# Optimization experiments

Hardware: AMD Instinct MI355X
Metric: run time of the kernel (lower is better)

The kernel has to match this reference:

```python
import jax, jax.numpy as jnp
import numpy as np

NUM_HEADS = 32
NUM_KV_HEADS = 8
HEAD_DIM = 128
SCALE = 1.0 / np.sqrt(HEAD_DIM)
BATCH = 16
MAX_CTX = 2048
NUM_SLOTS = BATCH * MAX_CTX + BATCH  # 32784; last BATCH slots are the write targets


def setup_inputs() -> dict:
    key = jax.random.key(0)
    ks = jax.random.split(key, 8)
    q = jax.random.normal(ks[0], (BATCH, NUM_HEADS, HEAD_DIM), dtype=jnp.float32)
    k = jax.random.normal(ks[1], (BATCH, NUM_KV_HEADS, HEAD_DIM), dtype=jnp.float32)
    v = jax.random.normal(ks[2], (BATCH, NUM_KV_HEADS, HEAD_DIM), dtype=jnp.float32)
    k_cache = jax.random.normal(ks[3], (NUM_SLOTS, NUM_KV_HEADS, HEAD_DIM), dtype=jnp.float32)
    v_cache = jax.random.normal(ks[4], (NUM_SLOTS, NUM_KV_HEADS, HEAD_DIM), dtype=jnp.float32)
    # each decode token writes its new kv into a fresh slot at the end of the pool
    slot_mapping = (BATCH * MAX_CTX + jnp.arange(BATCH)).astype(jnp.int64)
    # sparse-controller-selected active slots per request (paged, irregular)
    active_slots = jax.random.randint(ks[5], (BATCH, MAX_CTX), 0, NUM_SLOTS).astype(jnp.int64)
    # make the current token's slot the last active slot of its own request
    active_slots = active_slots.at[:, -1].set(slot_mapping)
    context_lens = jax.random.randint(ks[6], (BATCH,), 1, MAX_CTX + 1).astype(jnp.int64)
    return {
        "q": q, "k": k, "v": v,
        "k_cache": k_cache, "v_cache": v_cache,
        "slot_mapping": slot_mapping,
        "active_slots": active_slots,
        "context_lens": context_lens,
    }


def _attend(q, k, v, k_cache, v_cache, slot_mapping, active_slots, context_lens):
    # store_kvcache: scatter new k/v into flat slot cache; slot == -1 is skipped
    safe_slots = jnp.where(slot_mapping < 0, NUM_SLOTS, slot_mapping)  # OOB -> dropped
    kc = k_cache.at[safe_slots].set(k, mode="drop")
    vc = v_cache.at[safe_slots].set(v, mode="drop")

    # paged gather of the per-request active KV pages
    K = kc[active_slots]  # [B, L, Hkv, D]
    V = vc[active_slots]  # [B, L, Hkv, D]

    B, H, D = q.shape
    G = H // NUM_KV_HEADS  # GQA group size
    qg = q.reshape(B, NUM_KV_HEADS, G, D)

    # flash-decode stage1+stage2 == numerically-stable softmax attention over active slots
    scores = jnp.einsum("bkgd,blkd->bkgl", qg, K) * SCALE  # [B, Hkv, G, L]
    valid = jnp.arange(active_slots.shape[1])[None, :] < context_lens[:, None]  # [B, L]
    scores = jnp.where(valid[:, None, None, :], scores, jnp.float32(-1e30))
    p = jax.nn.softmax(scores, axis=-1)
    o = jnp.einsum("bkgl,blkd->bkgd", p, V).reshape(B, H, D)
    return o


def reference(q, k, v, k_cache, v_cache, slot_mapping, active_slots, context_lens):
    return _attend(q, k, v, k_cache, v_cache, slot_mapping, active_slots, context_lens)
```

## Files before the change

### kernel.cpp

```cpp
#include <hip/hip_runtime.h>
#include <hip/hip_bf16.h>
#include <float.h>

#define B 16
#define H 32
#define HKV 8
#define G 4
#define D 128
#define LMAX 2048
#define SCALE 0.08838834764831844f

template <int NSPLIT>
__global__ __launch_bounds__(256) void attn_partial(
    const float* __restrict__ q,
    const float* __restrict__ kin,
    const float* __restrict__ vin,
    const float* __restrict__ kc,
    const float* __restrict__ vc,
    const int*  __restrict__ slot_mapping,
    const int*  __restrict__ active_slots,
    const int*  __restrict__ context_lens,
    float* __restrict__ part_o,
    float* __restrict__ part_ml)
{
    constexpr int CHUNK = LMAX / NSPLIT;
    const int tid = threadIdx.x;
    int idx = blockIdx.x;
    const int split = idx % NSPLIT; idx /= NSPLIT;
    const int h = idx % HKV;
    const int b = idx / HKV;

    const int ctx   = context_lens[b];
    const int start = split * CHUNK;
    int nvalid = ctx - start;
    if (nvalid > CHUNK) nvalid = CHUNK;

    const size_t pbase = ((size_t)(b * HKV + h) * NSPLIT + split) * G;

    if (nvalid <= 0) {
        if (tid < G * 2) part_ml[pbase * 2 + tid] = (tid & 1) ? 0.f : -FLT_MAX;
        return;
    }

    __shared__ float sc[G][CHUNK];
    __shared__ const float* vptr[CHUNK];
    __shared__ float red[G][D];
    __shared__ int   sm[16];

    if (tid < 16) sm[tid] = slot_mapping[tid];
    __syncthreads();

    const int grp   = tid >> 3;
    const int lane8 = tid & 7;

    float4 qv[G][4];
#pragma unroll
    for (int g = 0; g < G; ++g) {
        const float* qp = q + ((size_t)(b * H + h * G + g)) * D;
#pragma unroll
        for (int i = 0; i < 4; ++i) {
            float4 t = *(const float4*)(qp + i * 32 + lane8 * 4);
            qv[g][i] = make_float4(t.x * SCALE, t.y * SCALE, t.z * SCALE, t.w * SCALE);
        }
    }

    const int iters = (nvalid + 31) >> 5;
    for (int it = 0; it < iters; ++it) {
        const int li = it * 32 + grp;
        if (li < nvalid) {
            const int l = start + li;
            const int s = active_slots[b * LMAX + l];
            int ov = -1;
#pragma unroll
            for (int j = 0; j < 16; ++j)
                if (sm[j] == s) ov = j;
            const float* kb = (ov >= 0) ? (kin + ((size_t)ov * HKV + h) * D)
                                        : (kc  + ((size_t)s  * HKV + h) * D);
            float pd0 = 0.f, pd1 = 0.f, pd2 = 0.f, pd3 = 0.f;
#pragma unroll
            for (int i = 0; i < 4; ++i) {
                float4 kv = *(const float4*)(kb + i * 32 + lane8 * 4);
                pd0 += kv.x * qv[0][i].x + kv.y * qv[0][i].y + kv.z * qv[0][i].z + kv.w * qv[0][i].w;
                pd1 += kv.x * qv[1][i].x + kv.y * qv[1][i].y + kv.z * qv[1][i].z + kv.w * qv[1][i].w;
                pd2 += kv.x * qv[2][i].x + kv.y * qv[2][i].y + kv.z * qv[2][i].z + kv.w * qv[2][i].w;
                pd3 += kv.x * qv[3][i].x + kv.y * qv[3][i].y + kv.z * qv[3][i].z + kv.w * qv[3][i].w;
            }
#pragma unroll
            for (int msk = 1; msk < 8; msk <<= 1) {
                pd0 += __shfl_xor(pd0, msk, 8);
                pd1 += __shfl_xor(pd1, msk, 8);
                pd2 += __shfl_xor(pd2, msk, 8);
                pd3 += __shfl_xor(pd3, msk, 8);
            }
            if (lane8 == 0) {
                sc[0][li] = pd0; sc[1][li] = pd1; sc[2][li] = pd2; sc[3][li] = pd3;
                vptr[li] = (ov >= 0) ? (vin + ((size_t)ov * HKV + h) * D)
                                     : (vc  + ((size_t)s  * HKV + h) * D);
            }
        }
    }
    __syncthreads();

    {
        const int g    = tid >> 6;
        const int lane = tid & 63;
        float m = -FLT_MAX;
        for (int i = lane; i < nvalid; i += 64) m = fmaxf(m, sc[g][i]);
#pragma unroll
        for (int msk = 1; msk < 64; msk <<= 1) m = fmaxf(m, __shfl_xor(m, msk, 64));
        float sum = 0.f;
        for (int i = lane; i < nvalid; i += 64) {
            float p = __expf(sc[g][i] - m);
            sc[g][i] = p;
            sum += p;
        }
#pragma unroll
        for (int msk = 1; msk < 64; msk <<= 1) sum += __shfl_xor(sum, msk, 64);
        if (lane == 0) {
            part_ml[(pbase + g) * 2 + 0] = m;
            part_ml[(pbase + g) * 2 + 1] = sum;
        }
    }
    __syncthreads();

    {
        const int dd   = tid & 127;
        const int half = tid >> 7;
        float a0 = 0.f, a1 = 0.f, a2 = 0.f, a3 = 0.f;
#pragma unroll 4
        for (int i = half; i < nvalid; i += 2) {
            const float* vb = vptr[i];
            const float vval = vb[dd];
            a0 += sc[0][i] * vval;
            a1 += sc[1][i] * vval;
            a2 += sc[2][i] * vval;
            a3 += sc[3][i] * vval;
        }
        if (half == 1) {
            red[0][dd] = a0; red[1][dd] = a1; red[2][dd] = a2; red[3][dd] = a3;
        }
        __syncthreads();
        if (half == 0) {
            part_o[(pbase + 0) * D + dd] = a0 + red[0][dd];
            part_o[(pbase + 1) * D + dd] = a1 + red[1][dd];
            part_o[(pbase + 2) * D + dd] = a2 + red[2][dd];
            part_o[(pbase + 3) * D + dd] = a3 + red[3][dd];
        }
    }
}

__global__ __launch_bounds__(128) void attn_reduce(
    const float* __restrict__ part_o,
    const float* __restrict__ part_ml,
    float* __restrict__ out,
    int nsplit)
{
    int idx = blockIdx.x;
    const int g = idx & 3;
    const int h = (idx >> 2) & 7;
    const int b = idx >> 5;
    const int d = threadIdx.x;

    const size_t base = (size_t)(b * HKV + h) * nsplit;

    float M = -FLT_MAX;
    for (int s = 0; s < nsplit; ++s) {
        const float l = part_ml[((base + s) * G + g) * 2 + 1];
        if (l > 0.f) M = fmaxf(M, part_ml[((base + s) * G + g) * 2 + 0]);
    }
    float L = 0.f, acc = 0.f;
    for (int s = 0; s < nsplit; ++s) {
        const float l = part_ml[((base + s) * G + g) * 2 + 1];
        if (l > 0.f) {
            const float e = __expf(part_ml[((base + s) * G + g) * 2 + 0] - M);
            L += l * e;
            acc += e * part_o[((base + s) * G + g) * D + d];
        }
    }
    out[((size_t)(b * H) + h * G + g) * D + d] = acc / (L > 0.f ? L : 1.f);
}

extern "C" void kernel_launch(void* const* d_in, const int* in_sizes, int n_in,
                              void* d_out, int out_size, void* d_ws, size_t ws_size,
                              hipStream_t stream) {
    const float* q  = (const float*)d_in[0];
    const float* k  = (const float*)d_in[1];
    const float* v  = (const float*)d_in[2];
    const float* kc = (const float*)d_in[3];
    const float* vc = (const float*)d_in[4];
    const int* slot_mapping = (const int*)d_in[5];
    const int* active_slots = (const int*)d_in[6];
    const int* context_lens = (const int*)d_in[7];
    float* out = (float*)d_out;

    const size_t need16 = ((size_t)B * HKV * 16 * G * D + (size_t)B * HKV * 16 * G * 2) * sizeof(float);
    const int nsplit = (ws_size >= need16) ? 16 : 8;

    float* part_o  = (float*)d_ws;
    float* part_ml = part_o + (size_t)B * HKV * nsplit * G * D;

    if (nsplit == 16) {
        attn_partial<16><<<B * HKV * 16, 256, 0, stream>>>(
            q, k, v, kc, vc, slot_mapping, active_slots, context_lens, part_o, part_ml);
    } else {
        attn_partial<8><<<B * HKV * 8, 256, 0, stream>>>(
            q, k, v, kc, vc, slot_mapping, active_slots, context_lens, part_o, part_ml);
    }
    attn_reduce<<<B * HKV * G, 128, 0, stream>>>(part_o, part_ml, out, nsplit);
}
```

Baseline: 48.57 us.

## Precompute slot pointers, vectorize PV accumulation, allow 32-way split-K

Slot lookup and the slot_mapping override check now run once per token in a separate prologue that stores K and V row pointers in shared memory, so the QK loop only loads K. The PV stage now has 8 token groups each doing float4 V loads across D, followed by an 8-way shared-memory reduction, in place of 2 halves doing scalar loads. The launcher also picks NSPLIT=32 when the workspace is large enough, giving more blocks and shorter chunks. This costs an extra barrier, more shared memory for the reduction buffer, and more partial results for the reduce kernel to combine.

```diff
diff --git a/kernel.cpp b/kernel.cpp
--- a/kernel.cpp
+++ b/kernel.cpp
@@ -43,11 +43,28 @@
     }
 
     __shared__ float sc[G][CHUNK];
-    __shared__ const float* vptr[CHUNK];
-    __shared__ float red[G][D];
+    __shared__ const float* kp[CHUNK];
+    __shared__ const float* vp[CHUNK];
+    __shared__ float red[8][G][D];
     __shared__ int   sm[16];
 
     if (tid < 16) sm[tid] = slot_mapping[tid];
+    __syncthreads();
+
+    for (int li = tid; li < nvalid; li += 256) {
+        const int s = active_slots[b * LMAX + start + li];
+        int ov = -1;
+#pragma unroll
+        for (int j = 0; j < 16; ++j)
+            if (sm[j] == s) ov = j;
+        if (ov >= 0) {
+            kp[li] = kin + ((size_t)ov * HKV + h) * D;
+            vp[li] = vin + ((size_t)ov * HKV + h) * D;
+        } else {
+            kp[li] = kc + ((size_t)s * HKV + h) * D;
+            vp[li] = vc + ((size_t)s * HKV + h) * D;
+        }
+    }
     __syncthreads();
 
     const int grp   = tid >> 3;
@@ -64,39 +81,26 @@
         }
     }
 
-    const int iters = (nvalid + 31) >> 5;
-    for (int it = 0; it < iters; ++it) {
-        const int li = it * 32 + grp;
-        if (li < nvalid) {
-            const int l = start + li;
-            const int s = active_slots[b * LMAX + l];
-            int ov = -1;
-#pragma unroll
-            for (int j = 0; j < 16; ++j)
-                if (sm[j] == s) ov = j;
-            const float* kb = (ov >= 0) ? (kin + ((size_t)ov * HKV + h) * D)
-                                        : (kc  + ((size_t)s  * HKV + h) * D);
-            float pd0 = 0.f, pd1 = 0.f, pd2 = 0.f, pd3 = 0.f;
-#pragma unroll
-            for (int i = 0; i < 4; ++i) {
-                float4 kv = *(const float4*)(kb + i * 32 + lane8 * 4);
-                pd0 += kv.x * qv[0][i].x + kv.y * qv[0][i].y + kv.z * qv[0][i].z + kv.w * qv[0][i].w;
-                pd1 += kv.x * qv[1][i].x + kv.y * qv[1][i].y + kv.z * qv[1][i].z + kv.w * qv[1][i].w;
-                pd2 += kv.x * qv[2][i].x + kv.y * qv[2][i].y + kv.z * qv[2][i].z + kv.w * qv[2][i].w;
-                pd3 += kv.x * qv[3][i].x + kv.y * qv[3][i].y + kv.z * qv[3][i].z + kv.w * qv[3][i].w;
-            }
-#pragma unroll
-            for (int msk = 1; msk < 8; msk <<= 1) {
-                pd0 += __shfl_xor(pd0, msk, 8);
-                pd1 += __shfl_xor(pd1, msk, 8);
-                pd2 += __shfl_xor(pd2, msk, 8);
-                pd3 += __shfl_xor(pd3, msk, 8);
-            }
-            if (lane8 == 0) {
-                sc[0][li] = pd0; sc[1][li] = pd1; sc[2][li] = pd2; sc[3][li] = pd3;
-                vptr[li] = (ov >= 0) ? (vin + ((size_t)ov * HKV + h) * D)
-                                     : (vc  + ((size_t)s  * HKV + h) * D);
-            }
+    for (int li = grp; li < nvalid; li += 32) {
+        const float* kb = kp[li];
+        float pd0 = 0.f, pd1 = 0.f, pd2 = 0.f, pd3 = 0.f;
+#pragma unroll
+        for (int i = 0; i < 4; ++i) {
+            float4 kv = *(const float4*)(kb + i * 32 + lane8 * 4);
+            pd0 += kv.x * qv[0][i].x + kv.y * qv[0][i].y + kv.z * qv[0][i].z + kv.w * qv[0][i].w;
+            pd1 += kv.x * qv[1][i].x + kv.y * qv[1][i].y + kv.z * qv[1][i].z + kv.w * qv[1][i].w;
+            pd2 += kv.x * qv[2][i].x + kv.y * qv[2][i].y + kv.z * qv[2][i].z + kv.w * qv[2][i].w;
+            pd3 += kv.x * qv[3][i].x + kv.y * qv[3][i].y + kv.z * qv[3][i].z + kv.w * qv[3][i].w;
+        }
+#pragma unroll
+        for (int msk = 1; msk < 8; msk <<= 1) {
+            pd0 += __shfl_xor(pd0, msk, 8);
+            pd1 += __shfl_xor(pd1, msk, 8);
+            pd2 += __shfl_xor(pd2, msk, 8);
+            pd3 += __shfl_xor(pd3, msk, 8);
+        }
+        if (lane8 == 0) {
+            sc[0][li] = pd0; sc[1][li] = pd1; sc[2][li] = pd2; sc[3][li] = pd3;
         }
     }
     __syncthreads();
@@ -124,27 +128,36 @@
     __syncthreads();
 
     {
-        const int dd   = tid & 127;
-        const int half = tid >> 7;
-        float a0 = 0.f, a1 = 0.f, a2 = 0.f, a3 = 0.f;
+        const int grp8  = tid >> 5;
+        const int dlane = tid & 31;
+        const int db    = dlane * 4;
+        float4 a0 = {0,0,0,0}, a1 = {0,0,0,0}, a2 = {0,0,0,0}, a3 = {0,0,0,0};
 #pragma unroll 4
-        for (int i = half; i < nvalid; i += 2) {
-            const float* vb = vptr[i];
-            const float vval = vb[dd];
-            a0 += sc[0][i] * vval;
-            a1 += sc[1][i] * vval;
-            a2 += sc[2][i] * vval;
-            a3 += sc[3][i] * vval;
-        }
-        if (half == 1) {
-            red[0][dd] = a0; red[1][dd] = a1; red[2][dd] = a2; red[3][dd] = a3;
-        }
-        __syncthreads();
-        if (half == 0) {
-            part_o[(pbase + 0) * D + dd] = a0 + red[0][dd];
-            part_o[(pbase + 1) * D + dd] = a1 + red[1][dd];
-            part_o[(pbase + 2) * D + dd] = a2 + red[2][dd];
-            part_o[(pbase + 3) * D + dd] = a3 + red[3][dd];
+        for (int i = grp8; i < nvalid; i += 8) {
+            const float4 vv = *(const float4*)(vp[i] + db);
+            const float p0 = sc[0][i], p1 = sc[1][i], p2 = sc[2][i], p3 = sc[3][i];
+            a0.x += p0 * vv.x; a0.y += p0 * vv.y; a0.z += p0 * vv.z; a0.w += p0 * vv.w;
+            a1.x += p1 * vv.x; a1.y += p1 * vv.y; a1.z += p1 * vv.z; a1.w += p1 * vv.w;
+            a2.x += p2 * vv.x; a2.y += p2 * vv.y; a2.z += p2 * vv.z; a2.w += p2 * vv.w;
+            a3.x += p3 * vv.x; a3.y += p3 * vv.y; a3.z += p3 * vv.z; a3.w += p3 * vv.w;
+        }
+        *(float4*)(&red[grp8][0][db]) = a0;
+        *(float4*)(&red[grp8][1][db]) = a1;
+        *(float4*)(&red[grp8][2][db]) = a2;
+        *(float4*)(&red[grp8][3][db]) = a3;
+    }
+    __syncthreads();
+
+    {
+#pragma unroll
+        for (int k2 = 0; k2 < 2; ++k2) {
+            const int oidx = tid * 2 + k2;
+            const int g = oidx >> 7;
+            const int d = oidx & 127;
+            float s = 0.f;
+#pragma unroll
+            for (int r = 0; r < 8; ++r) s += red[r][g][d];
+            part_o[(pbase + g) * D + d] = s;
         }
     }
 }
@@ -193,13 +206,18 @@
     const int* context_lens = (const int*)d_in[7];
     float* out = (float*)d_out;
 
-    const size_t need16 = ((size_t)B * HKV * 16 * G * D + (size_t)B * HKV * 16 * G * 2) * sizeof(float);
-    const int nsplit = (ws_size >= need16) ? 16 : 8;
+    const size_t perSplit = (size_t)B * HKV * (G * D + G * 2) * sizeof(float);
+    int nsplit = 8;
+    if (ws_size >= 32 * perSplit)      nsplit = 32;
+    else if (ws_size >= 16 * perSplit) nsplit = 16;
 
     float* part_o  = (float*)d_ws;
     float* part_ml = part_o + (size_t)B * HKV * nsplit * G * D;
 
-    if (nsplit == 16) {
+    if (nsplit == 32) {
+        attn_partial<32><<<B * HKV * 32, 256, 0, stream>>>(
+            q, k, v, kc, vc, slot_mapping, active_slots, context_lens, part_o, part_ml);
+    } else if (nsplit == 16) {
         attn_partial<16><<<B * HKV * 16, 256, 0, stream>>>(
             q, k, v, kc, vc, slot_mapping, active_slots, context_lens, part_o, part_ml);
     } else {
```

Result: no change. 49.50 us (+1.9%).

## Process all KV heads per block to read full contiguous slot rows

Applied to the files above, without the earlier changes.

Each attention-partial block now covers all 8 KV heads for one batch and context chunk, so the 256 threads read a whole 4 KB K/V slot row with float4 loads instead of a 512-byte per-head piece. Slot resolution happens once per token and is shared across heads. The context is split into many smaller chunks (up to 128 splits) chosen by workspace size. The reduce kernel stages per-split max/sum values in LDS. This should improve memory coalescing and avoid repeating index lookups per head. The cost is more partial outputs for the reduce kernel to merge and a serial per-token loop with 32-wide shuffle reductions.

```diff
diff --git a/kernel.cpp b/kernel.cpp
--- a/kernel.cpp
+++ b/kernel.cpp
@@ -10,7 +10,7 @@
 #define LMAX 2048
 #define SCALE 0.08838834764831844f
 
-template <int NSPLIT>
+template <int CHUNK>
 __global__ __launch_bounds__(256) void attn_partial(
     const float* __restrict__ q,
     const float* __restrict__ kin,
@@ -23,129 +23,112 @@
     float* __restrict__ part_o,
     float* __restrict__ part_ml)
 {
-    constexpr int CHUNK = LMAX / NSPLIT;
-    const int tid = threadIdx.x;
-    int idx = blockIdx.x;
-    const int split = idx % NSPLIT; idx /= NSPLIT;
-    const int h = idx % HKV;
-    const int b = idx / HKV;
+    constexpr int NSPLIT = LMAX / CHUNK;
+    const int tid   = threadIdx.x;
+    const int split = blockIdx.x % NSPLIT;
+    const int b     = blockIdx.x / NSPLIT;
 
     const int ctx   = context_lens[b];
     const int start = split * CHUNK;
     int nvalid = ctx - start;
     if (nvalid > CHUNK) nvalid = CHUNK;
 
-    const size_t pbase = ((size_t)(b * HKV + h) * NSPLIT + split) * G;
-
     if (nvalid <= 0) {
-        if (tid < G * 2) part_ml[pbase * 2 + tid] = (tid & 1) ? 0.f : -FLT_MAX;
+        if (tid < HKV * G * 2) {
+            const int h = tid >> 3, g = (tid >> 1) & 3, w = tid & 1;
+            part_ml[(((size_t)(b * HKV + h) * NSPLIT + split) * G + g) * 2 + w] =
+                w ? 0.f : -FLT_MAX;
+        }
         return;
     }
 
-    __shared__ float sc[G][CHUNK];
-    __shared__ const float* vptr[CHUNK];
-    __shared__ float red[G][D];
-    __shared__ int   sm[16];
+    __shared__ float sc[CHUNK][HKV * G];
+    __shared__ const float* kp[CHUNK];
+    __shared__ const float* vp[CHUNK];
+    __shared__ int sm[16];
 
     if (tid < 16) sm[tid] = slot_mapping[tid];
     __syncthreads();
 
-    const int grp   = tid >> 3;
-    const int lane8 = tid & 7;
-
-    float4 qv[G][4];
+    if (tid < CHUNK && tid < nvalid) {
+        const int s = active_slots[b * LMAX + start + tid];
+        int ov = -1;
+#pragma unroll
+        for (int j = 0; j < 16; ++j)
+            if (sm[j] == s) ov = j;
+        kp[tid] = (ov >= 0) ? kin + (size_t)ov * (HKV * D) : kc + (size_t)s * (HKV * D);
+        vp[tid] = (ov >= 0) ? vin + (size_t)ov * (HKV * D) : vc + (size_t)s * (HKV * D);
+    }
+
+    const int h  = tid >> 5;
+    const int db = (tid & 31) * 4;
+
+    float4 qv[G];
 #pragma unroll
     for (int g = 0; g < G; ++g) {
-        const float* qp = q + ((size_t)(b * H + h * G + g)) * D;
-#pragma unroll
-        for (int i = 0; i < 4; ++i) {
-            float4 t = *(const float4*)(qp + i * 32 + lane8 * 4);
-            qv[g][i] = make_float4(t.x * SCALE, t.y * SCALE, t.z * SCALE, t.w * SCALE);
-        }
-    }
-
-    const int iters = (nvalid + 31) >> 5;
-    for (int it = 0; it < iters; ++it) {
-        const int li = it * 32 + grp;
-        if (li < nvalid) {
-            const int l = start + li;
-            const int s = active_slots[b * LMAX + l];
-            int ov = -1;
-#pragma unroll
-            for (int j = 0; j < 16; ++j)
-                if (sm[j] == s) ov = j;
-            const float* kb = (ov >= 0) ? (kin + ((size_t)ov * HKV + h) * D)
-                                        : (kc  + ((size_t)s  * HKV + h) * D);
-            float pd0 = 0.f, pd1 = 0.f, pd2 = 0.f, pd3 = 0.f;
-#pragma unroll
-            for (int i = 0; i < 4; ++i) {
-                float4 kv = *(const float4*)(kb + i * 32 + lane8 * 4);
-                pd0 += kv.x * qv[0][i].x + kv.y * qv[0][i].y + kv.z * qv[0][i].z + kv.w * qv[0][i].w;
-                pd1 += kv.x * qv[1][i].x + kv.y * qv[1][i].y + kv.z * qv[1][i].z + kv.w * qv[1][i].w;
-                pd2 += kv.x * qv[2][i].x + kv.y * qv[2][i].y + kv.z * qv[2][i].z + kv.w * qv[2][i].w;
-                pd3 += kv.x * qv[3][i].x + kv.y * qv[3][i].y + kv.z * qv[3][i].z + kv.w * qv[3][i].w;
-            }
-#pragma unroll
-            for (int msk = 1; msk < 8; msk <<= 1) {
-                pd0 += __shfl_xor(pd0, msk, 8);
-                pd1 += __shfl_xor(pd1, msk, 8);
-                pd2 += __shfl_xor(pd2, msk, 8);
-                pd3 += __shfl_xor(pd3, msk, 8);
-            }
-            if (lane8 == 0) {
-                sc[0][li] = pd0; sc[1][li] = pd1; sc[2][li] = pd2; sc[3][li] = pd3;
-                vptr[li] = (ov >= 0) ? (vin + ((size_t)ov * HKV + h) * D)
-                                     : (vc  + ((size_t)s  * HKV + h) * D);
-            }
-        }
+        float4 t = *(const float4*)(q + ((size_t)(b * H + h * G + g)) * D + db);
+        qv[g] = make_float4(t.x * SCALE, t.y * SCALE, t.z * SCALE, t.w * SCALE);
+    }
+    __syncthreads();
+
+#pragma unroll 4
+    for (int i = 0; i < nvalid; ++i) {
+        const float4 kv = *(const float4*)(kp[i] + tid * 4);
+        float pd0 = kv.x * qv[0].x + kv.y * qv[0].y + kv.z * qv[0].z + kv.w * qv[0].w;
+        float pd1 = kv.x * qv[1].x + kv.y * qv[1].y + kv.z * qv[1].z + kv.w * qv[1].w;
+        float pd2 = kv.x * qv[2].x + kv.y * qv[2].y + kv.z * qv[2].z + kv.w * qv[2].w;
+        float pd3 = kv.x * qv[3].x + kv.y * qv[3].y + kv.z * qv[3].z + kv.w * qv[3].w;
+#pragma unroll
+        for (int msk = 1; msk < 32; msk <<= 1) {
+            pd0 += __shfl_xor(pd0, msk, 32);
+            pd1 += __shfl_xor(pd1, msk, 32);
+            pd2 += __shfl_xor(pd2, msk, 32);
+            pd3 += __shfl_xor(pd3, msk, 32);
+        }
+        if ((tid & 31) == 0)
+            *(float4*)&sc[i][h << 2] = make_float4(pd0, pd1, pd2, pd3);
     }
     __syncthreads();
 
     {
-        const int g    = tid >> 6;
-        const int lane = tid & 63;
+        const int r = tid >> 3, off = tid & 7;
         float m = -FLT_MAX;
-        for (int i = lane; i < nvalid; i += 64) m = fmaxf(m, sc[g][i]);
-#pragma unroll
-        for (int msk = 1; msk < 64; msk <<= 1) m = fmaxf(m, __shfl_xor(m, msk, 64));
+        for (int i = off; i < nvalid; i += 8) m = fmaxf(m, sc[i][r]);
+#pragma unroll
+        for (int msk = 1; msk < 8; msk <<= 1) m = fmaxf(m, __shfl_xor(m, msk, 8));
         float sum = 0.f;
-        for (int i = lane; i < nvalid; i += 64) {
-            float p = __expf(sc[g][i] - m);
-            sc[g][i] = p;
+        for (int i = off; i < nvalid; i += 8) {
+            const float p = __expf(sc[i][r] - m);
+            sc[i][r] = p;
             sum += p;
         }
 #pragma unroll
-        for (int msk = 1; msk < 64; msk <<= 1) sum += __shfl_xor(sum, msk, 64);
-        if (lane == 0) {
-            part_ml[(pbase + g) * 2 + 0] = m;
-            part_ml[(pbase + g) * 2 + 1] = sum;
-        }
-    }
-    __syncthreads();
-
+        for (int msk = 1; msk < 8; msk <<= 1) sum += __shfl_xor(sum, msk, 8);
+        if (off == 0) {
+            const int hh = r >> 2, g = r & 3;
+            const size_t mlb = (((size_t)(b * HKV + hh) * NSPLIT + split) * G + g) * 2;
+            part_ml[mlb + 0] = m;
+            part_ml[mlb + 1] = sum;
+        }
+    }
+    __syncthreads();
+
+    float4 a0 = {0,0,0,0}, a1 = {0,0,0,0}, a2 = {0,0,0,0}, a3 = {0,0,0,0};
+#pragma unroll 4
+    for (int i = 0; i < nvalid; ++i) {
+        const float4 vv = *(const float4*)(vp[i] + tid * 4);
+        const float4 p4 = *(const float4*)&sc[i][h << 2];
+        a0.x += p4.x * vv.x; a0.y += p4.x * vv.y; a0.z += p4.x * vv.z; a0.w += p4.x * vv.w;
+        a1.x += p4.y * vv.x; a1.y += p4.y * vv.y; a1.z += p4.y * vv.z; a1.w += p4.y * vv.w;
+        a2.x += p4.z * vv.x; a2.y += p4.z * vv.y; a2.z += p4.z * vv.z; a2.w += p4.z * vv.w;
+        a3.x += p4.w * vv.x; a3.y += p4.w * vv.y; a3.z += p4.w * vv.z; a3.w += p4.w * vv.w;
+    }
     {
-        const int dd   = tid & 127;
-        const int half = tid >> 7;
-        float a0 = 0.f, a1 = 0.f, a2 = 0.f, a3 = 0.f;
-#pragma unroll 4
-        for (int i = half; i < nvalid; i += 2) {
-            const float* vb = vptr[i];
-            const float vval = vb[dd];
-            a0 += sc[0][i] * vval;
-            a1 += sc[1][i] * vval;
-            a2 += sc[2][i] * vval;
-            a3 += sc[3][i] * vval;
-        }
-        if (half == 1) {
-            red[0][dd] = a0; red[1][dd] = a1; red[2][dd] = a2; red[3][dd] = a3;
-        }
-        __syncthreads();
-        if (half == 0) {
-            part_o[(pbase + 0) * D + dd] = a0 + red[0][dd];
-            part_o[(pbase + 1) * D + dd] = a1 + red[1][dd];
-            part_o[(pbase + 2) * D + dd] = a2 + red[2][dd];
-            part_o[(pbase + 3) * D + dd] = a3 + red[3][dd];
-        }
+        const size_t ob = ((size_t)(b * HKV + h) * NSPLIT + split) * G;
+        *(float4*)(part_o + (ob + 0) * D + db) = a0;
+        *(float4*)(part_o + (ob + 1) * D + db) = a1;
+        *(float4*)(part_o + (ob + 2) * D + db) = a2;
+        *(float4*)(part_o + (ob + 3) * D + db) = a3;
     }
 }
 
@@ -155,24 +138,29 @@
     float* __restrict__ out,
     int nsplit)
 {
-    int idx = blockIdx.x;
-    const int g = idx & 3;
-    const int h = (idx >> 2) & 7;
-    const int b = idx >> 5;
+    const int g = blockIdx.x & 3;
+    const int h = (blockIdx.x >> 2) & 7;
+    const int b = blockIdx.x >> 5;
     const int d = threadIdx.x;
 
+    __shared__ float mlds[128], llds[128];
     const size_t base = (size_t)(b * HKV + h) * nsplit;
 
+    for (int s = d; s < nsplit; s += 128) {
+        mlds[s] = part_ml[((base + s) * G + g) * 2 + 0];
+        llds[s] = part_ml[((base + s) * G + g) * 2 + 1];
+    }
+    __syncthreads();
+
     float M = -FLT_MAX;
-    for (int s = 0; s < nsplit; ++s) {
-        const float l = part_ml[((base + s) * G + g) * 2 + 1];
-        if (l > 0.f) M = fmaxf(M, part_ml[((base + s) * G + g) * 2 + 0]);
-    }
+    for (int s = 0; s < nsplit; ++s)
+        if (llds[s] > 0.f) M = fmaxf(M, mlds[s]);
+
     float L = 0.f, acc = 0.f;
     for (int s = 0; s < nsplit; ++s) {
-        const float l = part_ml[((base + s) * G + g) * 2 + 1];
+        const float l = llds[s];
         if (l > 0.f) {
-            const float e = __expf(part_ml[((base + s) * G + g) * 2 + 0] - M);
+            const float e = __expf(mlds[s] - M);
             L += l * e;
             acc += e * part_o[((base + s) * G + g) * D + d];
         }
@@ -193,17 +181,26 @@
     const int* context_lens = (const int*)d_in[7];
     float* out = (float*)d_out;
 
-    const size_t need16 = ((size_t)B * HKV * 16 * G * D + (size_t)B * HKV * 16 * G * 2) * sizeof(float);
-    const int nsplit = (ws_size >= need16) ? 16 : 8;
+    const size_t perSplit = (size_t)B * HKV * (G * D + G * 2) * sizeof(float);
+    int nsplit = 16;
+    if (ws_size >= 128 * perSplit)      nsplit = 128;
+    else if (ws_size >= 64 * perSplit)  nsplit = 64;
+    else if (ws_size >= 32 * perSplit)  nsplit = 32;
 
     float* part_o  = (float*)d_ws;
     float* part_ml = part_o + (size_t)B * HKV * nsplit * G * D;
 
-    if (nsplit == 16) {
-        attn_partial<16><<<B * HKV * 16, 256, 0, stream>>>(
+    if (nsplit == 128) {
+        attn_partial<16><<<B * 128, 256, 0, stream>>>(
+            q, k, v, kc, vc, slot_mapping, active_slots, context_lens, part_o, part_ml);
+    } else if (nsplit == 64) {
+        attn_partial<32><<<B * 64, 256, 0, stream>>>(
+            q, k, v, kc, vc, slot_mapping, active_slots, context_lens, part_o, part_ml);
+    } else if (nsplit == 32) {
+        attn_partial<64><<<B * 32, 256, 0, stream>>>(
             q, k, v, kc, vc, slot_mapping, active_slots, context_lens, part_o, part_ml);
     } else {
-        attn_partial<8><<<B * HKV * 8, 256, 0, stream>>>(
+        attn_partial<128><<<B * 16, 256, 0, stream>>>(
             q, k, v, kc, vc, slot_mapping, active_slots, context_lens, part_o, part_ml);
     }
     attn_reduce<<<B * HKV * G, 128, 0, stream>>>(part_o, part_ml, out, nsplit);
```

Measured after the change: 92.02 us. 89.5% more time.
